# Performance work log

Measured on AMD Instinct MI355X. Metric: run time of the kernel, lower is better.

## Reference

```python
import jax, jax.numpy as jnp
import numpy as np

KH, KW = 3, 3
STRIDE = (1, 1)
PADDING = (1, 1)
DILATION = (1, 1)


def setup_inputs() -> dict:
    key = jax.random.key(0)
    k1, k2, k3, k4, k5 = jax.random.split(key, 5)
    B, Cin, H, W = 8, 64, 128, 128
    Cout = 64
    Ho, Wo = 128, 128  # stride 1, pad 1, k=3 -> same spatial size
    K = KH * KW
    return {
        "input": jax.random.normal(k1, (B, Cin, H, W), dtype=jnp.float32),
        "offset": jax.random.normal(k2, (B, 2 * K, Ho, Wo), dtype=jnp.float32),
        "mask": jax.random.uniform(k3, (B, K, Ho, Wo), dtype=jnp.float32),
        "weight": jax.random.normal(k4, (Cout, Cin, KH, KW), dtype=jnp.float32) * 0.05,
        "bias": jax.random.normal(k5, (Cout,), dtype=jnp.float32) * 0.05,
    }


def _deform_conv2d(x, weight, offset, mask, bias, stride, padding, dilation):
    B, Cin, H, W = x.shape
    Cout, Cing, kh, kw = weight.shape
    G = Cin // Cing                      # weight groups
    K = kh * kw
    Goff = offset.shape[1] // (2 * K)    # offset groups
    Ho, Wo = offset.shape[2], offset.shape[3]
    Cg = Cin // Goff                     # channels per offset group
    sh, sw = stride
    ph, pw = padding
    dh, dw = dilation

    # offsets laid out as (y, x) pairs per kernel tap per offset group
    off = offset.reshape(B, Goff, K, 2, Ho, Wo)
    ky = (jnp.arange(K) // kw).astype(jnp.float32) * dh   # [K]
    kx = (jnp.arange(K) % kw).astype(jnp.float32) * dw
    gy = (jnp.arange(Ho).astype(jnp.float32) * sh - ph)    # [Ho]
    gx = (jnp.arange(Wo).astype(jnp.float32) * sw - pw)
    # sampling positions: [B, Goff, K, Ho, Wo]
    py = off[:, :, :, 0] + ky[None, None, :, None, None] + gy[None, None, None, :, None]
    px = off[:, :, :, 1] + kx[None, None, :, None, None] + gx[None, None, None, None, :]

    y0 = jnp.floor(py)
    x0 = jnp.floor(px)
    ly = py - y0
    lx = px - x0
    y0i = y0.astype(jnp.int32)
    x0i = x0.astype(jnp.int32)

    x_g = x.reshape(B, Goff, Cg, H * W)

    def gather(yi, xi):
        # zero padding outside the image
        valid = (yi >= 0) & (yi < H) & (xi >= 0) & (xi < W)
        yc = jnp.clip(yi, 0, H - 1)
        xc = jnp.clip(xi, 0, W - 1)
        idx = (yc * W + xc).reshape(B, Goff, K * Ho * Wo)
        v = jnp.take_along_axis(x_g, idx[:, :, None, :], axis=3)  # [B,Goff,Cg,K*Ho*Wo]
        return v * valid.reshape(B, Goff, 1, K * Ho * Wo)

    w00 = ((1 - ly) * (1 - lx)).reshape(B, Goff, 1, K * Ho * Wo)
    w01 = ((1 - ly) * lx).reshape(B, Goff, 1, K * Ho * Wo)
    w10 = (ly * (1 - lx)).reshape(B, Goff, 1, K * Ho * Wo)
    w11 = (ly * lx).reshape(B, Goff, 1, K * Ho * Wo)

    sampled = w00 * gather(y0i, x0i)
    sampled = sampled + w01 * gather(y0i, x0i + 1)
    sampled = sampled + w10 * gather(y0i + 1, x0i)
    sampled = sampled + w11 * gather(y0i + 1, x0i + 1)
    sampled = sampled.reshape(B, Goff, Cg, K, Ho, Wo)

    if mask is not None:
        sampled = sampled * mask.reshape(B, Goff, 1, K, Ho, Wo)

    # grouped conv accumulate
    sampled = sampled.reshape(B, G, Cing, K, Ho, Wo)
    w = weight.reshape(G, Cout // G, Cing, K)
    out = jnp.einsum('gock,bgcksq->bgosq', w, sampled).reshape(B, Cout, Ho, Wo)
    if bias is not None:
        out = out + bias[None, :, None, None]
    return out


def reference(input, offset, mask, weight, bias):
    return _deform_conv2d(input, weight, offset, mask, bias, STRIDE, PADDING, DILATION)
```

## Files before the change

kernel.cpp:

```cpp
#include <hip/hip_runtime.h>
#include <hip/hip_fp16.h>

#define HH 128
#define WW 128
#define HW (HH*WW)
#define XT_BYTES ((size_t)8 * HW * 64 * 2)
#define WT_BYTES ((size_t)9 * 2 * 4 * 64 * 8 * 2)

typedef __attribute__((ext_vector_type(8))) short short8;
typedef __attribute__((ext_vector_type(4))) float f32x4;
typedef _Float16 half8 __attribute__((ext_vector_type(8)));

static __device__ __forceinline__ unsigned short f2bf(float f) {
    unsigned int u = __float_as_uint(f);
    u += 0x7fffu + ((u >> 16) & 1u);
    return (unsigned short)(u >> 16);
}
static __device__ __forceinline__ unsigned pkrtz(float lo, float hi) {
    auto r = __builtin_amdgcn_cvt_pkrtz(lo, hi);
    return *(unsigned*)&r;
}

__global__ void wtrans_kernel(const float* __restrict__ w, unsigned short* __restrict__ wt) {
    int i = blockIdx.x * 256 + threadIdx.x;
    if (i < 9 * 2 * 4 * 64 * 8) {
        int e  = i & 7;
        int l  = (i >> 3) & 63;
        int wv = (i >> 9) & 3;
        int kf = (i >> 11) & 1;
        int k  = i >> 12;
        int co = wv * 16 + (l & 15);
        int c  = kf * 32 + (l >> 4) * 8 + e;
        __half hh = __float2half_rn(w[(co * 64 + c) * 9 + k]);
        wt[i] = __half_as_ushort(hh);
    }
}

__global__ __launch_bounds__(256) void xtrans_kernel(const float* __restrict__ x,
                                                     unsigned int* __restrict__ xt32) {
    __shared__ float tile[64][65];
    const int bid = blockIdx.x;
    const int b   = bid >> 8;
    const int hw0 = (bid & 255) << 6;
    const int t   = threadIdx.x;
    #pragma unroll
    for (int i = 0; i < 16; ++i) {
        int idx = (i << 8) + t;
        int c = idx >> 6, j = idx & 63;
        tile[c][j] = x[(size_t)(((b << 6) + c) << 14) + hw0 + j];
    }
    __syncthreads();
    #pragma unroll
    for (int i = 0; i < 8; ++i) {
        int idx = (i << 8) + t;
        int cp = idx & 31, hw = idx >> 5;
        xt32[((size_t)((b << 14) + hw0 + hw) << 5) + cp] =
            pkrtz(tile[2 * cp][hw], tile[2 * cp + 1][hw]);
    }
}

__global__ __launch_bounds__(256, 3) void deform_nhwc(
    const unsigned short* __restrict__ xt,
    const float* __restrict__ off,
    const float* __restrict__ msk,
    const unsigned short* __restrict__ wt,
    const float* __restrict__ bias,
    float* __restrict__ out)
{
    __shared__ __align__(16) unsigned char smem[25600];
    ushort4* moSu = (ushort4*)(smem + 16384);
    uint2*   mwH  = (uint2*)(smem + 20992);

    const int t   = threadIdx.x;
    const int bid = blockIdx.x;
    const int b   = bid & 7;
    const int rem = bid >> 3;
    const int ho  = rem >> 1;
    const int wo0 = (rem & 1) << 6;
    const int l   = t & 63;
    const int wv  = __builtin_amdgcn_readfirstlane(t >> 6);

    for (int i = t; i < 9 * 64; i += 256) {
        int p = i & 63;
        int k = i >> 6;
        int wo = wo0 + p;
        int obase = ((b * 18 + 2 * k) * HH + ho) * WW + wo;
        float oy = off[obase];
        float ox = off[obase + HW];
        float m  = msk[((b * 9 + k) * HH + ho) * WW + wo];
        float py = oy + (float)(k / 3) + (float)(ho - 1);
        float px = ox + (float)(k % 3) + (float)(wo - 1);
        float fy = floorf(py), fx = floorf(px);
        float ly = py - fy,    lx = px - fx;
        int y0 = (int)fy, x0 = (int)fx;
        int y1 = y0 + 1,  x1 = x0 + 1;
        float vy0 = (y0 >= 0 && y0 < HH) ? 1.f : 0.f;
        float vy1 = (y1 >= 0 && y1 < HH) ? 1.f : 0.f;
        float vx0 = (x0 >= 0 && x0 < WW) ? 1.f : 0.f;
        float vx1 = (x1 >= 0 && x1 < WW) ? 1.f : 0.f;
        float w00 = (1.f - ly) * (1.f - lx) * m * vy0 * vx0;
        float w01 = (1.f - ly) * lx         * m * vy0 * vx1;
        float w10 = ly         * (1.f - lx) * m * vy1 * vx0;
        float w11 = ly         * lx         * m * vy1 * vx1;
        int yc0 = min(max(y0, 0), HH - 1), yc1 = min(max(y1, 0), HH - 1);
        int xc0 = min(max(x0, 0), WW - 1), xc1 = min(max(x1, 0), WW - 1);
        moSu[i] = make_ushort4((unsigned short)(yc0 * WW + xc0),
                               (unsigned short)(yc0 * WW + xc1),
                               (unsigned short)(yc1 * WW + xc0),
                               (unsigned short)(yc1 * WW + xc1));
        __half2 hA = __floats2half2_rn(w00, w01);
        __half2 hB = __floats2half2_rn(w10, w11);
        mwH[i] = make_uint2(*(unsigned*)&hA, *(unsigned*)&hB);
    }

    const char* ib   = (const char*)xt + (size_t)b * HW * 128;
    const int  chb   = (l & 7) << 4;
    const int  px0_  = (wv << 4) + (l >> 3);
    int st_woff[2];
    st_woff[0] = px0_ * 128 + (chb ^ ((px0_ & 7) << 4));
    st_woff[1] = st_woff[0] + 8 * 128;
    const int lq = (l >> 4) << 4;
    const int sw = (l & 7) << 4;

    uint4 ga[8], gb[8];
    uint4 wtfu[2][2];

    #define GLD(dst, addr) \
        asm volatile("global_load_dwordx4 %0, %1, off" : "=v"(dst) : "v"(addr))

    #define GATHER(kk, A) {                                                  \
        ushort4 ob0 = moSu[(kk) * 64 + px0_];                                \
        ushort4 ob1 = moSu[(kk) * 64 + px0_ + 8];                            \
        GLD(A[0], (unsigned long long)(ib + (((int)ob0.x) << 7) + chb));     \
        GLD(A[1], (unsigned long long)(ib + (((int)ob0.y) << 7) + chb));     \
        GLD(A[2], (unsigned long long)(ib + (((int)ob0.z) << 7) + chb));     \
        GLD(A[3], (unsigned long long)(ib + (((int)ob0.w) << 7) + chb));     \
        GLD(A[4], (unsigned long long)(ib + (((int)ob1.x) << 7) + chb));     \
        GLD(A[5], (unsigned long long)(ib + (((int)ob1.y) << 7) + chb));     \
        GLD(A[6], (unsigned long long)(ib + (((int)ob1.z) << 7) + chb));     \
        GLD(A[7], (unsigned long long)(ib + (((int)ob1.w) << 7) + chb));     \
    }

    #define WTFLD(kk, idx) {                                                 \
        GLD(wtfu[idx][0], (unsigned long long)((const char*)wt + ((size_t)((((kk) * 2 + 0) * 4 + wv) * 64 + l) << 4))); \
        GLD(wtfu[idx][1], (unsigned long long)((const char*)wt + ((size_t)((((kk) * 2 + 1) * 4 + wv) * 64 + l) << 4))); \
    }

    #define VMCNT(n)  asm volatile("s_waitcnt vmcnt(" #n ")" ::: "memory"); \
                      __builtin_amdgcn_sched_barrier(0);
    #define STAGE_BARRIER() asm volatile("s_waitcnt lgkmcnt(0)" ::: "memory"); \
                            __builtin_amdgcn_s_barrier();

    #define CMBH(dst_, c00, c01, c10, c11) {                         \
        __half2 a_ = __hmul2(*(__half2*)&(c11), W11);                \
        a_ = __hfma2(*(__half2*)&(c10), W10, a_);                    \
        a_ = __hfma2(*(__half2*)&(c01), W01, a_);                    \
        a_ = __hfma2(*(__half2*)&(c00), W00, a_);                    \
        dst_ = *(unsigned*)&a_;                                      \
    }

    #define COMBINE_STORE(kk, A, dstb) {                             \
        {                                                            \
            uint2 wp = mwH[(kk) * 64 + px0_];                        \
            __half2 wab = *(__half2*)&wp.x, wcd = *(__half2*)&wp.y;  \
            __half2 W00 = __half2half2(__low2half(wab));             \
            __half2 W01 = __half2half2(__high2half(wab));            \
            __half2 W10 = __half2half2(__low2half(wcd));             \
            __half2 W11 = __half2half2(__high2half(wcd));            \
            uint4 uv;                                                \
            CMBH(uv.x, A[0].x, A[1].x, A[2].x, A[3].x)               \
            CMBH(uv.y, A[0].y, A[1].y, A[2].y, A[3].y)               \
            CMBH(uv.z, A[0].z, A[1].z, A[2].z, A[3].z)               \
            CMBH(uv.w, A[0].w, A[1].w, A[2].w, A[3].w)               \
            *(uint4*)((dstb) + st_woff[0]) = uv;                     \
        }                                                            \
        {                                                            \
            uint2 wp = mwH[(kk) * 64 + px0_ + 8];                    \
            __half2 wab = *(__half2*)&wp.x, wcd = *(__half2*)&wp.y;  \
            __half2 W00 = __half2half2(__low2half(wab));             \
            __half2 W01 = __half2half2(__high2half(wab));            \
            __half2 W10 = __half2half2(__low2half(wcd));             \
            __half2 W11 = __half2half2(__high2half(wcd));            \
            uint4 uv;                                                \
            CMBH(uv.x, A[4].x, A[5].x, A[6].x, A[7].x)               \
            CMBH(uv.y, A[4].y, A[5].y, A[6].y, A[7].y)               \
            CMBH(uv.z, A[4].z, A[5].z, A[6].z, A[7].z)               \
            CMBH(uv.w, A[4].w, A[5].w, A[6].w, A[7].w)               \
            *(uint4*)((dstb) + st_woff[1]) = uv;                     \
        }                                                            \
    }

    __syncthreads();

    GATHER(0, ga)
    WTFLD(0, 0)
    GATHER(1, gb)
    VMCNT(10)
    COMBINE_STORE(0, ga, smem)
    STAGE_BARRIER()

    f32x4 acc[4];
    #pragma unroll
    for (int g = 0; g < 4; ++g) acc[g] = (f32x4){0.f, 0.f, 0.f, 0.f};

    #pragma unroll
    for (int s = 0; s < 9; ++s) {
        if (s < 8) { VMCNT(8) } else { VMCNT(0) }
        {
            const unsigned char* rb = smem + ((s & 1) << 13);
            #pragma unroll
            for (int g = 0; g < 4; ++g) {
                const int prow = g * 16 + (l & 15);
                short8 a0 = *(const short8*)(rb + prow * 128 + (lq ^ sw));
                short8 a1 = *(const short8*)(rb + prow * 128 + ((64 + lq) ^ sw));
                acc[g] = __builtin_amdgcn_mfma_f32_16x16x32_f16(*(half8*)&a0, *(half8*)&wtfu[s & 1][0], acc[g], 0, 0, 0);
                acc[g] = __builtin_amdgcn_mfma_f32_16x16x32_f16(*(half8*)&a1, *(half8*)&wtfu[s & 1][1], acc[g], 0, 0, 0);
            }
        }
        if (s < 8) {
            WTFLD(s + 1, (s + 1) & 1)
            if ((s & 1) == 0) {
                if (s < 7) { GATHER(s + 2, ga) VMCNT(10) } else { VMCNT(2) }
                COMBINE_STORE(s + 1, gb, smem + (((s + 1) & 1) << 13))
            } else {
                if (s < 7) { GATHER(s + 2, gb) VMCNT(10) } else { VMCNT(2) }
                COMBINE_STORE(s + 1, ga, smem + (((s + 1) & 1) << 13))
            }
        }
        STAGE_BARRIER()
    }
    #undef GLD
    #undef GATHER
    #undef WTFLD
    #undef VMCNT
    #undef STAGE_BARRIER
    #undef CMBH
    #undef COMBINE_STORE

    float* out_t = (float*)smem;
    const int cb = wv << 4;
    const int co_e = cb + (l & 15);
    const float bv = bias[co_e];
    const int swE = (co_e & 15) << 4;
    #pragma unroll
    for (int g = 0; g < 4; ++g) {
        int pxb = (g << 6) + ((l >> 4) << 4);
        float4 v = make_float4(acc[g][0] + bv, acc[g][1] + bv, acc[g][2] + bv, acc[g][3] + bv);
        *(float4*)((unsigned char*)out_t + co_e * 256 + (pxb ^ swE)) = v;
    }
    __syncthreads();
    float* outb = out + (size_t)b * 64 * HW + (size_t)ho * WW + wo0;
    #pragma unroll
    for (int j = 0; j < 4; ++j) {
        int co   = (t >> 4) + (j << 4);
        int colb = (t & 15) << 4;
        float4 v = *(const float4*)((const unsigned char*)out_t + co * 256 + (colb ^ ((co & 15) << 4)));
        *(float4*)&outb[(size_t)co * HW + ((t & 15) << 2)] = v;
    }
}

__global__ __launch_bounds__(256, 4) void deform_fallback(
    const float* __restrict__ x, const float* __restrict__ off,
    const float* __restrict__ msk, const float* __restrict__ wraw,
    const float* __restrict__ bias, float* __restrict__ out)
{
    __shared__ unsigned short s_tile[2][64][68];
    __shared__ __align__(16) unsigned char meta_mem[18432];
    float4* mwS = (float4*)meta_mem;
    int4*   moS = (int4*)(meta_mem + 9216);
    float*  out_t = (float*)meta_mem;

    const int t   = threadIdx.x;
    const int bid = blockIdx.x;
    const int b   = bid & 7;
    const int rem = bid >> 3;
    const int ho  = rem >> 1;
    const int wo0 = (rem & 1) << 6;
    const int l   = t & 63;
    const int wv_id = __builtin_amdgcn_readfirstlane(t >> 6);
    const int c0  = wv_id << 4;
    const int cb  = wv_id << 4;

    short8 wtf[2][2];
    #pragma unroll
    for (int kf = 0; kf < 2; ++kf) {
        short8 f;
        int co = cb + (l & 15);
        int cbase = kf * 32 + (l >> 4) * 8;
        #pragma unroll
        for (int e = 0; e < 8; ++e) f[e] = (short)f2bf(wraw[(co * 64 + cbase + e) * 9 + 0]);
        wtf[0][kf] = f;
    }

    for (int i = t; i < 9 * 64; i += 256) {
        int p = i & 63;
        int k = i >> 6;
        int wo = wo0 + p;
        int obase = ((b * 18 + 2 * k) * HH + ho) * WW + wo;
        float oy = off[obase];
        float ox = off[obase + HW];
        float m  = msk[((b * 9 + k) * HH + ho) * WW + wo];
        float py = oy + (float)(k / 3) + (float)(ho - 1);
        float px = ox + (float)(k % 3) + (float)(wo - 1);
        float fy = floorf(py), fx = floorf(px);
        float ly = py - fy,    lx = px - fx;
        int y0 = (int)fy, x0 = (int)fx;
        int y1 = y0 + 1,  x1 = x0 + 1;
        float vy0 = (y0 >= 0 && y0 < HH) ? 1.f : 0.f;
        float vy1 = (y1 >= 0 && y1 < HH) ? 1.f : 0.f;
        float vx0 = (x0 >= 0 && x0 < WW) ? 1.f : 0.f;
        float vx1 = (x1 >= 0 && x1 < WW) ? 1.f : 0.f;
        float w00 = (1.f - ly) * (1.f - lx) * m * vy0 * vx0;
        float w01 = (1.f - ly) * lx         * m * vy0 * vx1;
        float w10 = ly         * (1.f - lx) * m * vy1 * vx0;
        float w11 = ly         * lx         * m * vy1 * vx1;
        int yc0 = min(max(y0, 0), HH - 1), yc1 = min(max(y1, 0), HH - 1);
        int xc0 = min(max(x0, 0), WW - 1), xc1 = min(max(x1, 0), WW - 1);
        mwS[i] = make_float4(w00, w01, w10, w11);
        moS[i] = make_int4(yc0 * WW + xc0, yc0 * WW + xc1,
                           yc1 * WW + xc0, yc1 * WW + xc1);
    }

    const int p = t & 63;
    const float* xb = x + (size_t)(b * 64 + c0) * HW;
    __syncthreads();

    {
        float4 wv = mwS[p];
        int4   ov = moS[p];
        const float* pc = xb;
        #pragma unroll
        for (int i = 0; i < 16; i += 4) {
            float v0 = wv.x * pc[ov.x] + wv.y * pc[ov.y] + wv.z * pc[ov.z] + wv.w * pc[ov.w]; pc += HW;
            float v1 = wv.x * pc[ov.x] + wv.y * pc[ov.y] + wv.z * pc[ov.z] + wv.w * pc[ov.w]; pc += HW;
            float v2 = wv.x * pc[ov.x] + wv.y * pc[ov.y] + wv.z * pc[ov.z] + wv.w * pc[ov.w]; pc += HW;
            float v3 = wv.x * pc[ov.x] + wv.y * pc[ov.y] + wv.z * pc[ov.z] + wv.w * pc[ov.w]; pc += HW;
            uint2 u;
            u.x = (unsigned)f2bf(v0) | ((unsigned)f2bf(v1) << 16);
            u.y = (unsigned)f2bf(v2) | ((unsigned)f2bf(v3) << 16);
            *(uint2*)&s_tile[0][p][c0 + i] = u;
        }
    }
    __syncthreads();

    f32x4 acc[4];
    #pragma unroll
    for (int g = 0; g < 4; ++g) acc[g] = (f32x4){0.f, 0.f, 0.f, 0.f};

    #pragma unroll
    for (int s = 0; s < 9; ++s) {
        if (s < 8) {
            const int kn = s + 1;
            #pragma unroll
            for (int kf = 0; kf < 2; ++kf) {
                short8 f;
                int co = cb + (l & 15);
                int cbase = kf * 32 + (l >> 4) * 8;
                #pragma unroll
                for (int e = 0; e < 8; ++e) f[e] = (short)f2bf(wraw[(co * 64 + cbase + e) * 9 + kn]);
                wtf[kn & 1][kf] = f;
            }
            float4 wv = mwS[kn * 64 + p];
            int4   ov = moS[kn * 64 + p];
            const float* pc = xb;
            #pragma unroll
            for (int i = 0; i < 16; i += 4) {
                float v0 = wv.x * pc[ov.x] + wv.y * pc[ov.y] + wv.z * pc[ov.z] + wv.w * pc[ov.w]; pc += HW;
                float v1 = wv.x * pc[ov.x] + wv.y * pc[ov.y] + wv.z * pc[ov.z] + wv.w * pc[ov.w]; pc += HW;
                float v2 = wv.x * pc[ov.x] + wv.y * pc[ov.y] + wv.z * pc[ov.z] + wv.w * pc[ov.w]; pc += HW;
                float v3 = wv.x * pc[ov.x] + wv.y * pc[ov.y] + wv.z * pc[ov.z] + wv.w * pc[ov.w]; pc += HW;
                uint2 u;
                u.x = (unsigned)f2bf(v0) | ((unsigned)f2bf(v1) << 16);
                u.y = (unsigned)f2bf(v2) | ((unsigned)f2bf(v3) << 16);
                *(uint2*)&s_tile[kn & 1][p][c0 + i] = u;
            }
        }
        #pragma unroll
        for (int g = 0; g < 4; ++g) {
            const int prow = g * 16 + (l & 15);
            const unsigned short* rp = &s_tile[s & 1][prow][(l >> 4) * 8];
            union { short8 v; unsigned long long q[2]; } ua0, ua1;
            ua0.q[0] = *(const unsigned long long*)(rp);
            ua0.q[1] = *(const unsigned long long*)(rp + 4);
            ua1.q[0] = *(const unsigned long long*)(rp + 32);
            ua1.q[1] = *(const unsigned long long*)(rp + 36);
            acc[g] = __builtin_amdgcn_mfma_f32_16x16x32_bf16(ua0.v, wtf[s & 1][0], acc[g], 0, 0, 0);
            acc[g] = __builtin_amdgcn_mfma_f32_16x16x32_bf16(ua1.v, wtf[s & 1][1], acc[g], 0, 0, 0);
        }
        __syncthreads();
    }

    const float bv = bias[cb + (l & 15)];
    #pragma unroll
    for (int g = 0; g < 4; ++g) {
        int co = cb + (l & 15);
        int pxb = g * 16 + (l >> 4) * 4;
        #pragma unroll
        for (int r = 0; r < 4; ++r)
            out_t[co * 68 + pxb + r] = acc[g][r] + bv;
    }
    __syncthreads();
    float* outb = out + (size_t)b * 64 * HW + (size_t)ho * WW + wo0;
    #pragma unroll
    for (int j = 0; j < 4; ++j) {
        int co  = (t >> 4) + j * 16;
        int px0 = (t & 15) << 2;
        float4 v = *(float4*)&out_t[co * 68 + px0];
        *(float4*)&outb[(size_t)co * HW + px0] = v;
    }
}

extern "C" void kernel_launch(void* const* d_in, const int* in_sizes, int n_in,
                              void* d_out, int out_size, void* d_ws, size_t ws_size,
                              hipStream_t stream) {
    const float* x    = (const float*)d_in[0];
    const float* off  = (const float*)d_in[1];
    const float* msk  = (const float*)d_in[2];
    const float* w    = (const float*)d_in[3];
    const float* bias = (const float*)d_in[4];
    float* out = (float*)d_out;

    const size_t need = XT_BYTES + WT_BYTES;
    if (d_ws != nullptr && ws_size >= need) {
        unsigned int*   xt32 = (unsigned int*)d_ws;
        unsigned short* wt   = (unsigned short*)((char*)d_ws + XT_BYTES);
        xtrans_kernel<<<2048, 256, 0, stream>>>(x, xt32);
        wtrans_kernel<<<144, 256, 0, stream>>>(w, wt);
        deform_nhwc<<<2048, 256, 0, stream>>>((const unsigned short*)xt32, off, msk, wt, bias, out);
    } else {
        deform_fallback<<<2048, 256, 0, stream>>>(x, off, msk, w, bias, out);
    }
}
```

Before: 47.98 us.

## Process two taps per pipeline stage with compiler-scheduled loads

Restructures the deformable conv main loop so each stage stages two kernel taps in shared memory (double-buffered 16KB halves) instead of one. This halves the number of barriers and gives 8 MFMAs per fragment per stage. It also replaces the hand-written inline-asm loads and explicit vmcnt waits with plain C++ loads and sched_barriers, leaving wait placement to the compiler. Shared memory grows from about 25KB to 42KB per block, which may cut occupancy below the launch-bound target of 3 blocks, and the compiler may serialise waits less tightly than the manual scheme.

```diff
diff --git a/kernel.cpp b/kernel.cpp
--- a/kernel.cpp
+++ b/kernel.cpp
@@ -67,9 +67,9 @@
     const float* __restrict__ bias,
     float* __restrict__ out)
 {
-    __shared__ __align__(16) unsigned char smem[25600];
-    ushort4* moSu = (ushort4*)(smem + 16384);
-    uint2*   mwH  = (uint2*)(smem + 20992);
+    __shared__ __align__(16) unsigned char smem[41984];
+    ushort4* moSu = (ushort4*)(smem + 32768);
+    uint2*   mwH  = (uint2*)(smem + 37376);
 
     const int t   = threadIdx.x;
     const int bid = blockIdx.x;
@@ -122,34 +122,29 @@
     const int lq = (l >> 4) << 4;
     const int sw = (l & 7) << 4;
 
-    uint4 ga[8], gb[8];
-    uint4 wtfu[2][2];
-
-    #define GLD(dst, addr) \
-        asm volatile("global_load_dwordx4 %0, %1, off" : "=v"(dst) : "v"(addr))
-
-    #define GATHER(kk, A) {                                                  \
-        ushort4 ob0 = moSu[(kk) * 64 + px0_];                                \
-        ushort4 ob1 = moSu[(kk) * 64 + px0_ + 8];                            \
-        GLD(A[0], (unsigned long long)(ib + (((int)ob0.x) << 7) + chb));     \
-        GLD(A[1], (unsigned long long)(ib + (((int)ob0.y) << 7) + chb));     \
-        GLD(A[2], (unsigned long long)(ib + (((int)ob0.z) << 7) + chb));     \
-        GLD(A[3], (unsigned long long)(ib + (((int)ob0.w) << 7) + chb));     \
-        GLD(A[4], (unsigned long long)(ib + (((int)ob1.x) << 7) + chb));     \
-        GLD(A[5], (unsigned long long)(ib + (((int)ob1.y) << 7) + chb));     \
-        GLD(A[6], (unsigned long long)(ib + (((int)ob1.z) << 7) + chb));     \
-        GLD(A[7], (unsigned long long)(ib + (((int)ob1.w) << 7) + chb));     \
-    }
-
-    #define WTFLD(kk, idx) {                                                 \
-        GLD(wtfu[idx][0], (unsigned long long)((const char*)wt + ((size_t)((((kk) * 2 + 0) * 4 + wv) * 64 + l) << 4))); \
-        GLD(wtfu[idx][1], (unsigned long long)((const char*)wt + ((size_t)((((kk) * 2 + 1) * 4 + wv) * 64 + l) << 4))); \
-    }
-
-    #define VMCNT(n)  asm volatile("s_waitcnt vmcnt(" #n ")" ::: "memory"); \
-                      __builtin_amdgcn_sched_barrier(0);
-    #define STAGE_BARRIER() asm volatile("s_waitcnt lgkmcnt(0)" ::: "memory"); \
-                            __builtin_amdgcn_s_barrier();
+    uint4 gA[8], gB[8];
+    half8 wtf[2][2][2];
+
+    #define ISSUE_TAP(kk, A) {                                       \
+        ushort4 ob0 = moSu[(kk) * 64 + px0_];                        \
+        A[0] = *(const uint4*)(ib + (((int)ob0.x) << 7) + chb);      \
+        A[1] = *(const uint4*)(ib + (((int)ob0.y) << 7) + chb);      \
+        A[2] = *(const uint4*)(ib + (((int)ob0.z) << 7) + chb);      \
+        A[3] = *(const uint4*)(ib + (((int)ob0.w) << 7) + chb);      \
+        ushort4 ob1 = moSu[(kk) * 64 + px0_ + 8];                    \
+        A[4] = *(const uint4*)(ib + (((int)ob1.x) << 7) + chb);      \
+        A[5] = *(const uint4*)(ib + (((int)ob1.y) << 7) + chb);      \
+        A[6] = *(const uint4*)(ib + (((int)ob1.z) << 7) + chb);      \
+        A[7] = *(const uint4*)(ib + (((int)ob1.w) << 7) + chb);      \
+    }
+
+    #define WTFLD(kk, sp) {                                          \
+        _Pragma("unroll")                                            \
+        for (int kf = 0; kf < 2; ++kf) {                             \
+            short8 sv = *(const short8*)(wt + ((((kk) * 2 + kf) * 4 + wv) * 64 + l) * 8); \
+            wtf[sp][(kk) & 1][kf] = *(half8*)&sv;                    \
+        }                                                            \
+    }
 
     #define CMBH(dst_, c00, c01, c10, c11) {                         \
         __half2 a_ = __hmul2(*(__half2*)&(c11), W11);                \
@@ -192,50 +187,74 @@
 
     __syncthreads();
 
-    GATHER(0, ga)
+    ISSUE_TAP(0, gA)
+    ISSUE_TAP(1, gB)
     WTFLD(0, 0)
-    GATHER(1, gb)
-    VMCNT(10)
-    COMBINE_STORE(0, ga, smem)
-    STAGE_BARRIER()
+    WTFLD(1, 0)
+    COMBINE_STORE(0, gA, smem)
+    COMBINE_STORE(1, gB, smem + 8192)
+    __syncthreads();
 
     f32x4 acc[4];
     #pragma unroll
     for (int g = 0; g < 4; ++g) acc[g] = (f32x4){0.f, 0.f, 0.f, 0.f};
 
     #pragma unroll
-    for (int s = 0; s < 9; ++s) {
-        if (s < 8) { VMCNT(8) } else { VMCNT(0) }
+    for (int st = 0; st < 4; ++st) {
+        if (st < 3) {
+            ISSUE_TAP(2 * st + 2, gA)
+            ISSUE_TAP(2 * st + 3, gB)
+            WTFLD(2 * st + 2, (st + 1) & 1)
+            WTFLD(2 * st + 3, (st + 1) & 1)
+        } else {
+            ISSUE_TAP(8, gA)
+            WTFLD(8, (st + 1) & 1)
+        }
+        __builtin_amdgcn_sched_barrier(0);
         {
-            const unsigned char* rb = smem + ((s & 1) << 13);
+            const unsigned char* rb = smem + ((st & 1) << 14);
             #pragma unroll
             for (int g = 0; g < 4; ++g) {
                 const int prow = g * 16 + (l & 15);
-                short8 a0 = *(const short8*)(rb + prow * 128 + (lq ^ sw));
-                short8 a1 = *(const short8*)(rb + prow * 128 + ((64 + lq) ^ sw));
-                acc[g] = __builtin_amdgcn_mfma_f32_16x16x32_f16(*(half8*)&a0, *(half8*)&wtfu[s & 1][0], acc[g], 0, 0, 0);
-                acc[g] = __builtin_amdgcn_mfma_f32_16x16x32_f16(*(half8*)&a1, *(half8*)&wtfu[s & 1][1], acc[g], 0, 0, 0);
+                short8 a00 = *(const short8*)(rb + prow * 128 + (lq ^ sw));
+                short8 a01 = *(const short8*)(rb + prow * 128 + ((64 + lq) ^ sw));
+                short8 a10 = *(const short8*)(rb + 8192 + prow * 128 + (lq ^ sw));
+                short8 a11 = *(const short8*)(rb + 8192 + prow * 128 + ((64 + lq) ^ sw));
+                acc[g] = __builtin_amdgcn_mfma_f32_16x16x32_f16(*(half8*)&a00, wtf[st & 1][0][0], acc[g], 0, 0, 0);
+                acc[g] = __builtin_amdgcn_mfma_f32_16x16x32_f16(*(half8*)&a01, wtf[st & 1][0][1], acc[g], 0, 0, 0);
+                acc[g] = __builtin_amdgcn_mfma_f32_16x16x32_f16(*(half8*)&a10, wtf[st & 1][1][0], acc[g], 0, 0, 0);
+                acc[g] = __builtin_amdgcn_mfma_f32_16x16x32_f16(*(half8*)&a11, wtf[st & 1][1][1], acc[g], 0, 0, 0);
             }
         }
-        if (s < 8) {
-            WTFLD(s + 1, (s + 1) & 1)
-            if ((s & 1) == 0) {
-                if (s < 7) { GATHER(s + 2, ga) VMCNT(10) } else { VMCNT(2) }
-                COMBINE_STORE(s + 1, gb, smem + (((s + 1) & 1) << 13))
+        __builtin_amdgcn_sched_barrier(0);
+        {
+            unsigned char* wb = smem + (((st + 1) & 1) << 14);
+            if (st < 3) {
+                COMBINE_STORE(2 * st + 2, gA, wb)
+                COMBINE_STORE(2 * st + 3, gB, wb + 8192)
             } else {
-                if (s < 7) { GATHER(s + 2, gb) VMCNT(10) } else { VMCNT(2) }
-                COMBINE_STORE(s + 1, ga, smem + (((s + 1) & 1) << 13))
+                COMBINE_STORE(8, gA, wb)
             }
         }
-        STAGE_BARRIER()
-    }
-    #undef GLD
-    #undef GATHER
+        __syncthreads();
+    }
+    {
+        const unsigned char* rb = smem;
+        #pragma unroll
+        for (int g = 0; g < 4; ++g) {
+            const int prow = g * 16 + (l & 15);
+            short8 a00 = *(const short8*)(rb + prow * 128 + (lq ^ sw));
+            short8 a01 = *(const short8*)(rb + prow * 128 + ((64 + lq) ^ sw));
+            acc[g] = __builtin_amdgcn_mfma_f32_16x16x32_f16(*(half8*)&a00, wtf[0][0][0], acc[g], 0, 0, 0);
+            acc[g] = __builtin_amdgcn_mfma_f32_16x16x32_f16(*(half8*)&a01, wtf[0][0][1], acc[g], 0, 0, 0);
+        }
+    }
+    #undef ISSUE_TAP
     #undef WTFLD
-    #undef VMCNT
-    #undef STAGE_BARRIER
     #undef CMBH
     #undef COMBINE_STORE
+
+    __syncthreads();
 
     float* out_t = (float*)smem;
     const int cb = wv << 4;
```

New measurement: 49.05 us. 1.02x slower.
